# Kernel tuning notes

Hardware: AMD Instinct MI355X
Metric: run time of the kernel (lower is better)

Reference implementation:

```python
import jax, jax.numpy as jnp
import numpy as np

N = 12000   # nodes (multiple of 120)
E = 192000  # edges
T = 120     # utterances per dialogue
IN = 192
OUT = 6


def _edge_softmax(logits, dst, n):
    # logits: [E, H] -> softmax over incoming edges of each dst node
    m = jax.ops.segment_max(logits, dst, num_segments=n)
    ex = jnp.exp(logits - m[dst])
    s = jax.ops.segment_sum(ex, dst, num_segments=n)
    return ex / s[dst]


def _gatv2(h, src, dst, Wsrc, bsrc, Wdst, bdst, attn, Wres, n):
    # DGL GATv2Conv: e = attn . leakyrelu(fc_src(h)[u] + fc_dst(h)[v]), residual, relu activation
    Hh, F = attn.shape
    fs = (h @ Wsrc + bsrc).reshape(n, Hh, F)
    fd = (h @ Wdst + bdst).reshape(n, Hh, F)
    e = jax.nn.leaky_relu(fs[src] + fd[dst], 0.2)          # [E, H, F]
    logits = jnp.einsum('ehf,hf->eh', e, attn)              # [E, H]
    alpha = _edge_softmax(logits, dst, n)                   # [E, H]
    out = jax.ops.segment_sum(alpha[:, :, None] * fs[src], dst, num_segments=n)
    res = (h @ Wres).reshape(n, Hh, F)
    return jax.nn.relu(out + res)                           # [N, H, F]


def _lstm_dir(x, Wih, Whh, bih, bhh, reverse):
    # x: [T, B, D]; torch gate order i, f, g, o
    B = x.shape[1]
    hid = Whh.shape[1]
    def step(carry, xt):
        h, c = carry
        z = xt @ Wih.T + h @ Whh.T + bih + bhh
        i, f, g, o = jnp.split(z, 4, axis=-1)
        c = jax.nn.sigmoid(f) * c + jax.nn.sigmoid(i) * jnp.tanh(g)
        h = jax.nn.sigmoid(o) * jnp.tanh(c)
        return (h, c), h
    init = (jnp.zeros((B, hid), x.dtype), jnp.zeros((B, hid), x.dtype))
    _, hs = jax.lax.scan(step, init, x, reverse=reverse)
    return hs


def setup_inputs() -> dict:
    key = jax.random.key(0)
    ks = iter(jax.random.split(key, 64))
    def rn(shape, s=0.05):
        return jax.random.normal(next(ks), shape, jnp.float32) * s
    inp = {
        'text': rn((N, 1024), 1.0),
        'audio': rn((N, 512), 1.0),
        'vision': rn((N, 1024), 1.0),
        'edge_src': jax.random.randint(next(ks), (E,), 0, N, jnp.int32),
        'edge_dst': jax.random.randint(next(ks), (E,), 0, N, jnp.int32),
        # modality encoders
        'W_audio': rn((512, 64)), 'b_audio': jnp.zeros((64,), jnp.float32),
        'W_vision': rn((1024, 64)), 'b_vision': jnp.zeros((64,), jnp.float32),
        'W_text': rn((1024, 64)), 'b_text': jnp.zeros((64,), jnp.float32),
        # bidirectional LSTM (hidden=4 -> 16 gate rows)
        'Wih_f': rn((16, IN)), 'Whh_f': rn((16, 4)), 'bih_f': jnp.zeros((16,), jnp.float32), 'bhh_f': jnp.zeros((16,), jnp.float32),
        'Wih_b': rn((16, IN)), 'Whh_b': rn((16, 4)), 'bih_b': jnp.zeros((16,), jnp.float32), 'bhh_b': jnp.zeros((16,), jnp.float32),
        # imputation GraphConv (192->192, norm='both')
        'W_gc': rn((IN, IN)), 'b_gc': jnp.zeros((IN,), jnp.float32),
        # gat2 (cross-modal multi-head GAT, 192 -> 16 heads x 4)
        'Wsrc2': rn((IN, 64)), 'bsrc2': jnp.zeros((64,), jnp.float32),
        'Wdst2': rn((IN, 64)), 'bdst2': jnp.zeros((64,), jnp.float32),
        'attn2': rn((16, 4)), 'Wres2': rn((IN, 64)),
        # gat1 layer 0 (192 -> 16 heads x 32)
        'Wsrc0': rn((IN, 512)), 'bsrc0': jnp.zeros((512,), jnp.float32),
        'Wdst0': rn((IN, 512)), 'bdst0': jnp.zeros((512,), jnp.float32),
        'attn0': rn((16, 32)), 'Wres0': rn((IN, 512)),
        # gat1 layer 1 (512 -> 16 heads x 4)
        'Wsrc1': rn((512, 64)), 'bsrc1': jnp.zeros((64,), jnp.float32),
        'Wdst1': rn((512, 64)), 'bdst1': jnp.zeros((64,), jnp.float32),
        'attn1': rn((16, 4)), 'Wres1': rn((512, 64)),
        # final classifier Linear(136, out_size)
        'W_lin': rn((136, OUT)), 'b_lin': jnp.zeros((OUT,), jnp.float32),
    }
    return inp


def reference(text, audio, vision, edge_src, edge_dst,
              W_audio, b_audio, W_vision, b_vision, W_text, b_text,
              Wih_f, Whh_f, bih_f, bhh_f, Wih_b, Whh_b, bih_b, bhh_b,
              W_gc, b_gc,
              Wsrc2, bsrc2, Wdst2, bdst2, attn2, Wres2,
              Wsrc0, bsrc0, Wdst0, bdst0, attn0, Wres0,
              Wsrc1, bsrc1, Wdst1, bdst1, attn1, Wres1,
              W_lin, b_lin):
    n = text.shape[0]
    # modality encoders (dropout is identity at inference)
    t = text @ W_text + b_text
    a = audio @ W_audio + b_audio
    v = vision @ W_vision + b_vision
    stackFT = jnp.concatenate([t, a, v], axis=1)            # [N, 192]

    # bidirectional LSTM over dialogues of length T=120
    x = stackFT.reshape(-1, T, IN).transpose(1, 0, 2)       # [T, B, 192]
    hf = _lstm_dir(x, Wih_f, Whh_f, bih_f, bhh_f, False)
    hb = _lstm_dir(x, Wih_b, Whh_b, bih_b, bhh_b, True)
    newFeature = jnp.concatenate([hf, hb], -1).transpose(1, 0, 2).reshape(n, 8)

    # GraphConv imputation, norm='both' (degrees clamped to 1 as in DGL)
    ones = jnp.ones((edge_src.shape[0],), stackFT.dtype)
    deg_out = jnp.maximum(jax.ops.segment_sum(ones, edge_src, num_segments=n), 1.0)
    deg_in = jnp.maximum(jax.ops.segment_sum(ones, edge_dst, num_segments=n), 1.0)
    hw = (stackFT @ W_gc) * (deg_out ** -0.5)[:, None]
    h1 = jax.ops.segment_sum(hw[edge_src], edge_dst, num_segments=n) * (deg_in ** -0.5)[:, None] + b_gc
    h = 0.5 * (stackFT + h1)
    # F.normalize(h, p=1)
    h = h / jnp.maximum(jnp.sum(jnp.abs(h), axis=1, keepdims=True), 1e-12)

    # cross-modal multi-head GAT branch -> [N, 64]
    h3 = _gatv2(h, edge_src, edge_dst, Wsrc2, bsrc2, Wdst2, bdst2, attn2, Wres2, n).reshape(n, -1)

    # stacked GATv2 layers
    h = _gatv2(h, edge_src, edge_dst, Wsrc0, bsrc0, Wdst0, bdst0, attn0, Wres0, n).reshape(n, -1)  # [N, 512]
    h = _gatv2(h, edge_src, edge_dst, Wsrc1, bsrc1, Wdst1, bdst1, attn1, Wres1, n).reshape(n, -1)  # [N, 64]

    out = jnp.concatenate([h, newFeature, h3], axis=1) @ W_lin + b_lin  # [N, out_size]
    return out
```

## Files before the change

kernel.cpp:

```cpp
#include <hip/hip_runtime.h>

typedef __attribute__((ext_vector_type(8))) short short8;
typedef __attribute__((ext_vector_type(4))) float f32x4;

__device__ __forceinline__ unsigned short f2bf(float f) {
    unsigned u = __float_as_uint(f);
    u += 0x7FFFu + ((u >> 16) & 1u);
    return (unsigned short)(u >> 16);
}
__device__ __forceinline__ float bf2f(unsigned short h) {
    return __uint_as_float((unsigned)h << 16);
}

template<int MF, int OUTMODE>
__global__ __launch_bounds__(256)
void gemm_v6(const unsigned short* __restrict__ A, const float* __restrict__ B,
             const float* __restrict__ bias, const float* __restrict__ rowscale,
             void* __restrict__ Cv, const float* __restrict__ fin_num,
             const float* __restrict__ fin_den,
             int M, int Nb, int K, int ldc)
{
    __shared__ alignas(16) unsigned short As[MF * 64 * 32];
    __shared__ alignas(16) unsigned short Bs[4 * 64 * 8];
    const int t = threadIdx.x;
    const int w = t >> 6, l = t & 63;
    const int r16 = l & 15, kg = l >> 4;
    const int row0 = blockIdx.x * (64 * MF);
    const int col0 = blockIdx.y * 64;
    const int bcol = t & 63, bkg = t >> 6;

    f32x4 acc[MF][4] = {};
    const short8 z8 = {0, 0, 0, 0, 0, 0, 0, 0};

    for (int k0 = 0; k0 < K; k0 += 32) {
#pragma unroll
        for (int it = 0; it < MF; ++it) {
            int idx = it * 256 + t;
            int row = idx >> 2, ch = idx & 3;
            int gm = row0 + row;
            short8 v = z8;
            if (gm < M) v = *reinterpret_cast<const short8*>(A + (size_t)gm * K + k0 + ch * 8);
            *reinterpret_cast<short8*>(&As[row * 32 + ch * 8]) = v;
        }
        {
            const float* bp = B + (size_t)(k0 + bkg * 8) * Nb + col0 + bcol;
            short8 hv;
#pragma unroll
            for (int j = 0; j < 8; ++j) hv[j] = (short)f2bf(bp[(size_t)j * Nb]);
            *reinterpret_cast<short8*>(&Bs[bkg * 512 + bcol * 8]) = hv;
        }
        __syncthreads();
        short8 af[MF];
#pragma unroll
        for (int mi = 0; mi < MF; ++mi)
            af[mi] = *reinterpret_cast<const short8*>(&As[((w * MF + mi) * 16 + r16) * 32 + kg * 8]);
#pragma unroll
        for (int ni = 0; ni < 4; ++ni) {
            short8 bf = *reinterpret_cast<const short8*>(&Bs[kg * 512 + (ni * 16 + r16) * 8]);
#pragma unroll
            for (int mi = 0; mi < MF; ++mi)
                acc[mi][ni] = __builtin_amdgcn_mfma_f32_16x16x32_bf16(af[mi], bf, acc[mi][ni], 0, 0, 0);
        }
        __syncthreads();
    }
#pragma unroll
    for (int mi = 0; mi < MF; ++mi)
#pragma unroll
        for (int ni = 0; ni < 4; ++ni) {
            int col = col0 + ni * 16 + r16;
            float bv = bias ? bias[col] : 0.f;
#pragma unroll
            for (int r = 0; r < 4; ++r) {
                int gm = row0 + (w * MF + mi) * 16 + kg * 4 + r;
                if (gm < M) {
                    float val = acc[mi][ni][r] + bv;
                    if (rowscale) val *= rowscale[gm];
                    size_t idx = (size_t)gm * ldc + col;
                    if (OUTMODE == 0) {
                        ((float*)Cv)[idx] = val;
                    } else if (OUTMODE == 1) {
                        ((unsigned short*)Cv)[idx] = f2bf(val);
                    } else {
                        float d = fin_den[(size_t)gm * 16 + (col >> 5)];
                        float inv = (d > 0.f) ? __fdividef(1.f, d) : 0.f;
                        float o = fmaxf(fin_num[idx] * inv + val, 0.f);
                        ((unsigned short*)Cv)[idx] = f2bf(o);
                    }
                }
            }
        }
}

__global__ __launch_bounds__(256)
void enc_mfma3(const float* __restrict__ text, const float* __restrict__ audio, const float* __restrict__ vision,
               const float* __restrict__ Wt, const float* __restrict__ Wa, const float* __restrict__ Wv,
               const float* __restrict__ bt, const float* __restrict__ ba, const float* __restrict__ bv,
               float* __restrict__ Cf, unsigned short* __restrict__ Cb, int M)
{
    __shared__ alignas(16) unsigned short Ah[32 * 32], Ao[32 * 32];
    __shared__ alignas(16) unsigned short Bh[4 * 64 * 8], Bo[4 * 64 * 8];
    const int z = blockIdx.z;
    const float* A  = (z == 0) ? text : (z == 1) ? audio : vision;
    const float* W  = (z == 0) ? Wt   : (z == 1) ? Wa    : Wv;
    const float* bb = (z == 0) ? bt   : (z == 1) ? ba    : bv;
    const int K = (z == 1) ? 512 : 1024;

    const int t = threadIdx.x;
    const int w = t >> 6, l = t & 63;
    const int r16 = l & 15, kg = l >> 4;
    const int row0 = blockIdx.x * 32;
    const int mi = w & 1;
    const int ncol0 = (w >> 1) * 32;
    const int arow = t >> 3, ac8 = t & 7;
    const int bcol = t & 63, bkg = t >> 6;

    f32x4 acc[2] = {};
    for (int k0 = 0; k0 < K; k0 += 32) {
        {
            float4 av = *reinterpret_cast<const float4*>(A + (size_t)(row0 + arow) * K + k0 + ac8 * 4);
            float vv[4] = {av.x, av.y, av.z, av.w};
            ushort4 hi, lo;
            unsigned short* hp = (unsigned short*)&hi;
            unsigned short* lp = (unsigned short*)&lo;
#pragma unroll
            for (int j = 0; j < 4; ++j) {
                unsigned short h = f2bf(vv[j]);
                hp[j] = h;
                lp[j] = f2bf(vv[j] - bf2f(h));
            }
            *reinterpret_cast<ushort4*>(&Ah[arow * 32 + ac8 * 4]) = hi;
            *reinterpret_cast<ushort4*>(&Ao[arow * 32 + ac8 * 4]) = lo;
        }
        {
            const float* bp = W + (size_t)(k0 + bkg * 8) * 64 + bcol;
            short8 hv, lv;
#pragma unroll
            for (int j = 0; j < 8; ++j) {
                float x = bp[(size_t)j * 64];
                unsigned short h = f2bf(x);
                hv[j] = (short)h;
                lv[j] = (short)f2bf(x - bf2f(h));
            }
            *reinterpret_cast<short8*>(&Bh[bkg * 512 + bcol * 8]) = hv;
            *reinterpret_cast<short8*>(&Bo[bkg * 512 + bcol * 8]) = lv;
        }
        __syncthreads();
        short8 ah = *reinterpret_cast<const short8*>(&Ah[(mi * 16 + r16) * 32 + kg * 8]);
        short8 ao = *reinterpret_cast<const short8*>(&Ao[(mi * 16 + r16) * 32 + kg * 8]);
#pragma unroll
        for (int ni = 0; ni < 2; ++ni) {
            int ci = kg * 512 + (ncol0 + ni * 16 + r16) * 8;
            short8 bhv = *reinterpret_cast<const short8*>(&Bh[ci]);
            short8 bov = *reinterpret_cast<const short8*>(&Bo[ci]);
            acc[ni] = __builtin_amdgcn_mfma_f32_16x16x32_bf16(ah, bhv, acc[ni], 0, 0, 0);
            acc[ni] = __builtin_amdgcn_mfma_f32_16x16x32_bf16(ah, bov, acc[ni], 0, 0, 0);
            acc[ni] = __builtin_amdgcn_mfma_f32_16x16x32_bf16(ao, bhv, acc[ni], 0, 0, 0);
        }
        __syncthreads();
    }
#pragma unroll
    for (int ni = 0; ni < 2; ++ni) {
        int col = ncol0 + ni * 16 + r16;
        float bvv = bb[col];
#pragma unroll
        for (int r = 0; r < 4; ++r) {
            int gr = row0 + mi * 16 + kg * 4 + r;
            if (gr < M) {
                float val = acc[ni][r] + bvv;
                size_t idx = (size_t)gr * 192 + z * 64 + col;
                Cf[idx] = val;
                Cb[idx] = f2bf(val);
            }
        }
    }
}

__global__ void pack3_kernel(const float* __restrict__ W0, const float* __restrict__ W1, const float* __restrict__ W2,
                             const float* __restrict__ b0, const float* __restrict__ b1,
                             float* __restrict__ Wp, float* __restrict__ bp, int K, int O)
{
    int gid = blockIdx.x * blockDim.x + threadIdx.x;
    int O3 = 3 * O;
    if (gid < O3) bp[gid] = (gid < O) ? b0[gid] : (gid < 2 * O) ? b1[gid - O] : 0.f;
    if (gid >= K * O3) return;
    int k = gid / O3, c = gid - k * O3;
    float v = (c < O) ? W0[k * O + c] : (c < 2 * O) ? W1[k * O + c - O] : W2[k * O + c - 2 * O];
    Wp[gid] = v;
}

__global__ void pack2_kernel(const float* __restrict__ W0, const float* __restrict__ W1,
                             const float* __restrict__ b0, const float* __restrict__ b1,
                             float* __restrict__ Wp, float* __restrict__ bp, int K, int O)
{
    int gid = blockIdx.x * blockDim.x + threadIdx.x;
    int O2 = 2 * O;
    if (gid < O2) bp[gid] = (gid < O) ? b0[gid] : b1[gid - O];
    if (gid >= K * O2) return;
    int k = gid / O2, c = gid - k * O2;
    Wp[gid] = (c < O) ? W0[k * O + c] : W1[k * O + c - O];
}

__global__ void deg_kernel(const int* __restrict__ src, const int* __restrict__ dst,
                           int* degout, int* degin, int E)
{
    int e = blockIdx.x * blockDim.x + threadIdx.x;
    if (e < E) {
        atomicAdd(&degout[src[e]], 1);
        atomicAdd(&degin[dst[e]], 1);
    }
}

__global__ __launch_bounds__(1024)
void scan_kernel(const int* __restrict__ degin, int* __restrict__ rowstart, int n)
{
    __shared__ int part[1024];
    int t = threadIdx.x;
    int chunk = (n + 1023) / 1024;
    int s = 0;
    for (int i = 0; i < chunk; ++i) {
        int idx = t * chunk + i;
        if (idx < n) s += degin[idx];
    }
    part[t] = s;
    __syncthreads();
    for (int o = 1; o < 1024; o <<= 1) {
        int v = (t >= o) ? part[t - o] : 0;
        __syncthreads();
        part[t] += v;
        __syncthreads();
    }
    int run = (t > 0) ? part[t - 1] : 0;
    for (int i = 0; i < chunk; ++i) {
        int idx = t * chunk + i;
        if (idx < n) { rowstart[idx] = run; run += degin[idx]; }
    }
    if (t == 1023) rowstart[n] = part[1023];
}

__global__ void perm_kernel(const int* __restrict__ dst, const int* __restrict__ rowstart,
                            int* cursor, int* __restrict__ perm, int E)
{
    int e = blockIdx.x * blockDim.x + threadIdx.x;
    if (e < E) {
        int v = dst[e];
        int p = atomicAdd(&cursor[v], 1);
        perm[rowstart[v] + p] = e;
    }
}

__global__ void gather_src_kernel(const int* __restrict__ esrc, int* perm, int E)
{
    int i = blockIdx.x * blockDim.x + threadIdx.x;
    if (i < E) perm[i] = esrc[perm[i]];
}

__global__ void rs_kernel(const int* degout, const int* degin, float* rso, float* rsi, int n)
{
    int i = blockIdx.x * blockDim.x + threadIdx.x;
    if (i < n) {
        rso[i] = rsqrtf((float)max(degout[i], 1));
        rsi[i] = rsqrtf((float)max(degin[i], 1));
    }
}

__global__ void lstm_pre(const float* __restrict__ x, const float* __restrict__ Wf,
                         const float* __restrict__ Wb,
                         const float* bf1, const float* bf2, const float* bb1, const float* bb2,
                         float* __restrict__ xWf, float* __restrict__ xWb, int n)
{
    int gid = blockIdx.x * blockDim.x + threadIdx.x;
    if (gid >= n * 32) return;
    int nn = gid >> 5, r = gid & 31, d = r >> 4, j = r & 15;
    const float* W = (d ? Wb : Wf) + j * 192;
    const float* xr = x + (size_t)nn * 192;
    float s = 0.f;
#pragma unroll 4
    for (int k = 0; k < 192; k += 4) {
        float4 xv = *reinterpret_cast<const float4*>(xr + k);
        float4 wv = *reinterpret_cast<const float4*>(W + k);
        s += xv.x * wv.x + xv.y * wv.y + xv.z * wv.z + xv.w * wv.w;
    }
    s += d ? (bb1[j] + bb2[j]) : (bf1[j] + bf2[j]);
    int b = nn / 120, tt = nn - b * 120;
    (d ? xWb : xWf)[((size_t)b * 16 + j) * 120 + tt] = s;
}

__device__ __forceinline__ float fsigm(float x) { return __fdividef(1.f, 1.f + __expf(-x)); }
__device__ __forceinline__ float ftanh(float x) { return 1.f - __fdividef(2.f, __expf(2.f * x) + 1.f); }

template<int DIR>
__device__ void lstm_chain(const float* __restrict__ xw, const float* __restrict__ whh,
                           float* __restrict__ newF, int b)
{
    int j = threadIdx.x & 15;
    int k = j & 3;
    float4 w = *reinterpret_cast<const float4*>(whh + j * 4);
    const float* xp = xw + ((size_t)b * 16 + j) * 120;
    float h0 = 0.f, h1 = 0.f, h2 = 0.f, h3 = 0.f, cst = 0.f;
    int tb0 = DIR ? 108 : 0;
    float4 a0 = *reinterpret_cast<const float4*>(xp + tb0);
    float4 a1 = *reinterpret_cast<const float4*>(xp + tb0 + 4);
    float4 a2 = *reinterpret_cast<const float4*>(xp + tb0 + 8);
    for (int ch = 0; ch < 10; ++ch) {
        float4 b0 = a0, b1 = a1, b2 = a2;
        if (ch < 9) {
            int nt = DIR ? (96 - ch * 12) : (12 + ch * 12);
            b0 = *reinterpret_cast<const float4*>(xp + nt);
            b1 = *reinterpret_cast<const float4*>(xp + nt + 4);
            b2 = *reinterpret_cast<const float4*>(xp + nt + 8);
        }
        float zz[12] = {a0.x, a0.y, a0.z, a0.w, a1.x, a1.y, a1.z, a1.w, a2.x, a2.y, a2.z, a2.w};
        int tbase = DIR ? (108 - ch * 12) : (ch * 12);
#pragma unroll
        for (int ii = 0; ii < 12; ++ii) {
            int idx = DIR ? (11 - ii) : ii;
            float z = zz[idx] + ((w.x * h0 + w.y * h1) + (w.z * h2 + w.w * h3));
            float zi = __shfl(z, k, 16);
            float zf = __shfl(z, k + 4, 16);
            float zg = __shfl(z, k + 8, 16);
            float zo = __shfl(z, k + 12, 16);
            float ig = fsigm(zi), fg = fsigm(zf), gg = ftanh(zg), og = fsigm(zo);
            cst = fg * cst + ig * gg;
            float hn = og * ftanh(cst);
            h0 = __shfl(hn, 0, 16); h1 = __shfl(hn, 1, 16);
            h2 = __shfl(hn, 2, 16); h3 = __shfl(hn, 3, 16);
            if (j < 4) newF[((size_t)b * 120 + tbase + idx) * 8 + DIR * 4 + j] = hn;
        }
        a0 = b0; a1 = b1; a2 = b2;
    }
}

__global__ __launch_bounds__(64)
void lstm_seq2(const float* __restrict__ xWf, const float* __restrict__ xWb,
               const float* __restrict__ Whhf, const float* __restrict__ Whhb,
               float* __restrict__ newF, int B)
{
    int sub = threadIdx.x >> 4;
    int chain = blockIdx.x * 4 + sub;
    if (chain >= 2 * B) return;
    int d = chain / B;
    int b = chain - d * B;
    if (d == 0) lstm_chain<0>(xWf, Whhf, newF, b);
    else        lstm_chain<1>(xWb, Whhb, newF, b);
}

__global__ __launch_bounds__(256)
void gc_combine3(const float* __restrict__ stackFT, const float* __restrict__ hw,
                 const int* __restrict__ rowstart, const int* __restrict__ csrc,
                 const float* __restrict__ rs_in,
                 const float* __restrict__ b_gc, unsigned short* __restrict__ hB, int n)
{
    int v = blockIdx.x * 4 + (threadIdx.x >> 6);
    int l = threadIdx.x & 63;
    if (v >= n) return;
    int s0 = rowstart[v], s1 = rowstart[v + 1];
    float sum0 = 0.f, sum1 = 0.f, sum2 = 0.f;
    int u = (s0 < s1) ? csrc[s0] : 0;
    for (int i = s0; i < s1; ++i) {
        int un = (i + 1 < s1) ? csrc[i + 1] : 0;
        const float* hr = hw + (size_t)u * 192 + l;
        float p0 = hr[0], p1 = hr[64], p2 = hr[128];
        sum0 += p0; sum1 += p1; sum2 += p2;
        u = un;
    }
    float ri = rs_in[v];
    const float* sf = stackFT + (size_t)v * 192 + l;
    float v0 = 0.5f * (sf[0]   + sum0 * ri + b_gc[l]);
    float v1 = 0.5f * (sf[64]  + sum1 * ri + b_gc[l + 64]);
    float v2 = 0.5f * (sf[128] + sum2 * ri + b_gc[l + 128]);
    float r = fabsf(v0) + fabsf(v1) + fabsf(v2);
#pragma unroll
    for (int o = 32; o; o >>= 1) r += __shfl_xor(r, o);
    float inv = __fdividef(1.f, fmaxf(r, 1e-12f));
    unsigned short* hp = hB + (size_t)v * 192 + l;
    hp[0]   = f2bf(v0 * inv);
    hp[64]  = f2bf(v1 * inv);
    hp[128] = f2bf(v2 * inv);
}

__global__ __launch_bounds__(256)
void gat_edge4(const float* __restrict__ base, int ld,
               const float* __restrict__ attn,
               const int* __restrict__ rowstart, const int* __restrict__ csrc,
               float* __restrict__ outp, int n)
{
    int v = blockIdx.x * 16 + (threadIdx.x >> 4);
    int l = threadIdx.x & 15;
    if (v >= n) return;
    float4 at  = *reinterpret_cast<const float4*>(attn + l * 4);
    float4 fdv = *reinterpret_cast<const float4*>(base + (size_t)v * ld + 64 + l * 4);
    float4 acc = make_float4(0.f, 0.f, 0.f, 0.f);
    float dn = 0.f;
    int s0 = rowstart[v], s1 = rowstart[v + 1];
    int u = (s0 < s1) ? csrc[s0] : 0;
    float4 sv = (s0 < s1) ? *reinterpret_cast<const float4*>(base + (size_t)u * ld + l * 4)
                          : make_float4(0.f, 0.f, 0.f, 0.f);
    for (int i = s0; i < s1; ++i) {
        int un = (i + 1 < s1) ? csrc[i + 1] : 0;
        float4 svn = (i + 1 < s1) ? *reinterpret_cast<const float4*>(base + (size_t)un * ld + l * 4)
                                  : make_float4(0.f, 0.f, 0.f, 0.f);
        float ex_, ey, ez, ew;
        ex_ = sv.x + fdv.x; ex_ = (ex_ > 0.f) ? ex_ : 0.2f * ex_;
        ey  = sv.y + fdv.y; ey  = (ey  > 0.f) ? ey  : 0.2f * ey;
        ez  = sv.z + fdv.z; ez  = (ez  > 0.f) ? ez  : 0.2f * ez;
        ew  = sv.w + fdv.w; ew  = (ew  > 0.f) ? ew  : 0.2f * ew;
        float p = ex_ * at.x + ey * at.y + ez * at.z + ew * at.w;
        float ex = __expf(p);
        acc.x += ex * sv.x; acc.y += ex * sv.y; acc.z += ex * sv.z; acc.w += ex * sv.w;
        dn += ex;
        sv = svn; u = un;
    }
    float4 r = *reinterpret_cast<const float4*>(base + (size_t)v * ld + 128 + l * 4);
    float inv = (dn > 0.f) ? __fdividef(1.f, dn) : 0.f;
    float4 o;
    o.x = fmaxf(acc.x * inv + r.x, 0.f);
    o.y = fmaxf(acc.y * inv + r.y, 0.f);
    o.z = fmaxf(acc.z * inv + r.z, 0.f);
    o.w = fmaxf(acc.w * inv + r.w, 0.f);
    *reinterpret_cast<float4*>(outp + (size_t)v * 64 + l * 4) = o;
}

__global__ __launch_bounds__(256)
void gat_edge32(const unsigned short* __restrict__ base,
                const float* __restrict__ attn,
                const int* __restrict__ rowstart, const int* __restrict__ csrc,
                float* __restrict__ num, float* __restrict__ den, int n)
{
    int v = blockIdx.x * 2 + (threadIdx.x >> 7);
    int l = threadIdx.x & 127;
    if (v >= n) return;
    int head = l >> 3;
    float4 at = *reinterpret_cast<const float4*>(attn + head * 32 + (l & 7) * 4);
    ushort4 fdu = *reinterpret_cast<const ushort4*>(base + (size_t)v * 1024 + 512 + l * 4);
    float4 fdv = make_float4(bf2f(fdu.x), bf2f(fdu.y), bf2f(fdu.z), bf2f(fdu.w));
    float4 acc = make_float4(0.f, 0.f, 0.f, 0.f);
    float dn = 0.f;
    int s0 = rowstart[v], s1 = rowstart[v + 1];
    int u = (s0 < s1) ? csrc[s0] : 0;
    ushort4 su = (s0 < s1) ? *reinterpret_cast<const ushort4*>(base + (size_t)u * 1024 + l * 4)
                           : make_ushort4(0, 0, 0, 0);
    for (int i = s0; i < s1; ++i) {
        int un = (i + 1 < s1) ? csrc[i + 1] : 0;
        ushort4 sun = (i + 1 < s1) ? *reinterpret_cast<const ushort4*>(base + (size_t)un * 1024 + l * 4)
                                   : make_ushort4(0, 0, 0, 0);
        float4 sv = make_float4(bf2f(su.x), bf2f(su.y), bf2f(su.z), bf2f(su.w));
        float ex_, ey, ez, ew;
        ex_ = sv.x + fdv.x; ex_ = (ex_ > 0.f) ? ex_ : 0.2f * ex_;
        ey  = sv.y + fdv.y; ey  = (ey  > 0.f) ? ey  : 0.2f * ey;
        ez  = sv.z + fdv.z; ez  = (ez  > 0.f) ? ez  : 0.2f * ez;
        ew  = sv.w + fdv.w; ew  = (ew  > 0.f) ? ew  : 0.2f * ew;
        float p = ex_ * at.x + ey * at.y + ez * at.z + ew * at.w;
        p += __shfl_xor(p, 1, 8);
        p += __shfl_xor(p, 2, 8);
        p += __shfl_xor(p, 4, 8);
        float ex = __expf(p);
        acc.x += ex * sv.x; acc.y += ex * sv.y; acc.z += ex * sv.z; acc.w += ex * sv.w;
        dn += ex;
        su = sun; u = un;
    }
    *reinterpret_cast<float4*>(num + (size_t)v * 512 + l * 4) = acc;
    if ((l & 7) == 0) den[(size_t)v * 16 + head] = dn;
}

__global__ void final_lin(const float* __restrict__ h1, const float* __restrict__ newF,
                          const float* __restrict__ h3, const float* __restrict__ W,
                          const float* __restrict__ bias, float* __restrict__ out, int n)
{
    int gid = blockIdx.x * blockDim.x + threadIdx.x;
    if (gid >= n * 6) return;
    int v = gid / 6, o = gid - v * 6;
    float s = bias[o];
    const float* a = h1 + (size_t)v * 64;
#pragma unroll 8
    for (int r = 0; r < 64; ++r) s += a[r] * W[r * 6 + o];
    const float* b = newF + (size_t)v * 8;
#pragma unroll
    for (int r = 0; r < 8; ++r) s += b[r] * W[(64 + r) * 6 + o];
    const float* c = h3 + (size_t)v * 64;
#pragma unroll 8
    for (int r = 0; r < 64; ++r) s += c[r] * W[(72 + r) * 6 + o];
    out[gid] = s;
}

extern "C" void kernel_launch(void* const* d_in, const int* in_sizes, int n_in,
                              void* d_out, int out_size, void* d_ws, size_t ws_size,
                              hipStream_t stream)
{
    const float* text   = (const float*)d_in[0];
    const float* audio  = (const float*)d_in[1];
    const float* vision = (const float*)d_in[2];
    const int*   esrc   = (const int*)d_in[3];
    const int*   edst   = (const int*)d_in[4];
    const float* W_audio = (const float*)d_in[5];  const float* b_audio = (const float*)d_in[6];
    const float* W_vision= (const float*)d_in[7];  const float* b_vision= (const float*)d_in[8];
    const float* W_text  = (const float*)d_in[9];  const float* b_text  = (const float*)d_in[10];
    const float* Wih_f = (const float*)d_in[11]; const float* Whh_f = (const float*)d_in[12];
    const float* bih_f = (const float*)d_in[13]; const float* bhh_f = (const float*)d_in[14];
    const float* Wih_b = (const float*)d_in[15]; const float* Whh_b = (const float*)d_in[16];
    const float* bih_b = (const float*)d_in[17]; const float* bhh_b = (const float*)d_in[18];
    const float* W_gc  = (const float*)d_in[19]; const float* b_gc  = (const float*)d_in[20];
    const float* Wsrc2 = (const float*)d_in[21]; const float* bsrc2 = (const float*)d_in[22];
    const float* Wdst2 = (const float*)d_in[23]; const float* bdst2 = (const float*)d_in[24];
    const float* attn2 = (const float*)d_in[25]; const float* Wres2 = (const float*)d_in[26];
    const float* Wsrc0 = (const float*)d_in[27]; const float* bsrc0 = (const float*)d_in[28];
    const float* Wdst0 = (const float*)d_in[29]; const float* bdst0 = (const float*)d_in[30];
    const float* attn0 = (const float*)d_in[31]; const float* Wres0 = (const float*)d_in[32];
    const float* Wsrc1 = (const float*)d_in[33]; const float* bsrc1 = (const float*)d_in[34];
    const float* Wdst1 = (const float*)d_in[35]; const float* bdst1 = (const float*)d_in[36];
    const float* attn1 = (const float*)d_in[37]; const float* Wres1 = (const float*)d_in[38];
    const float* W_lin = (const float*)d_in[39]; const float* b_lin = (const float*)d_in[40];
    float* out = (float*)d_out;

    const int n = in_sizes[0] / 1024;
    const int E = in_sizes[3];
    const int B = n / 120;

    char* p = (char*)d_ws;
    auto alloc_f = [&](size_t cnt) { float* r = (float*)p; p += ((cnt * 4 + 255) / 256) * 256; return r; };
    auto alloc_h = [&](size_t cnt) { unsigned short* r = (unsigned short*)p; p += ((cnt * 2 + 255) / 256) * 256; return r; };
    auto alloc_i = [&](size_t cnt) { int* r = (int*)p; p += ((cnt * 4 + 255) / 256) * 256; return r; };
    float*          stackFT = alloc_f((size_t)n * 192);
    unsigned short* stackBF = alloc_h((size_t)n * 192);
    unsigned short* hbufBF  = alloc_h((size_t)n * 192);
    float* xWf     = alloc_f((size_t)n * 16);
    float* xWb     = alloc_f((size_t)n * 16);
    float* newF    = alloc_f((size_t)n * 8);
    float* big0    = alloc_f((size_t)n * 512);
    float* big1    = alloc_f((size_t)n * 512);
    float* big2    = alloc_f((size_t)n * 512);
    float* den     = alloc_f((size_t)n * 16);
    float* h3      = alloc_f((size_t)n * 64);
    float* h1s     = alloc_f((size_t)n * 64);
    float* rs_out  = alloc_f(n);
    float* rs_in   = alloc_f(n);
    int* zero_base = alloc_i((size_t)3 * n);
    int* degout = zero_base;
    int* degin  = zero_base + n;
    int* cursor = zero_base + 2 * n;
    int* rowstart = alloc_i((size_t)n + 1);
    int* perm     = alloc_i((size_t)E);
    if ((size_t)(p - (char*)d_ws) > ws_size) return;

    float* pw = h1s;
    float* pb = h1s + 200704;

    hipMemsetAsync(zero_base, 0, (size_t)3 * n * 4, stream);
    deg_kernel<<<(E + 255) / 256, 256, 0, stream>>>(esrc, edst, degout, degin, E);
    scan_kernel<<<1, 1024, 0, stream>>>(degin, rowstart, n);
    perm_kernel<<<(E + 255) / 256, 256, 0, stream>>>(edst, rowstart, cursor, perm, E);
    gather_src_kernel<<<(E + 255) / 256, 256, 0, stream>>>(esrc, perm, E);
    rs_kernel<<<(n + 255) / 256, 256, 0, stream>>>(degout, degin, rs_out, rs_in, n);
    const int* csrc = perm;

    auto gemm = [&](auto mf_tag, auto om_tag, const unsigned short* A, const float* Bm,
                    const float* bias, const float* rsc, void* Cp,
                    const float* fnum, const float* fden, int M, int Nb, int K, int ldc) {
        constexpr int MF = decltype(mf_tag)::value;
        constexpr int OM = decltype(om_tag)::value;
        dim3 grid((M + 64 * MF - 1) / (64 * MF), Nb / 64);
        gemm_v6<MF, OM><<<grid, 256, 0, stream>>>(A, Bm, bias, rsc, Cp, fnum, fden, M, Nb, K, ldc);
    };
    using I1 = std::integral_constant<int, 1>;
    using I2 = std::integral_constant<int, 2>;
    using O0 = std::integral_constant<int, 0>;
    using O1 = std::integral_constant<int, 1>;
    using O2 = std::integral_constant<int, 2>;

    {
        dim3 grid(n / 32, 1, 3);
        enc_mfma3<<<grid, 256, 0, stream>>>(text, audio, vision, W_text, W_audio, W_vision,
                                            b_text, b_audio, b_vision, stackFT, stackBF, n);
    }

    lstm_pre<<<(n * 32 + 255) / 256, 256, 0, stream>>>(stackFT, Wih_f, Wih_b,
                                                       bih_f, bhh_f, bih_b, bhh_b, xWf, xWb, n);
    lstm_seq2<<<(2 * B + 3) / 4, 64, 0, stream>>>(xWf, xWb, Whh_f, Whh_b, newF, B);

    gemm(I1{}, O0{}, stackBF, W_gc, nullptr, rs_out, big0, nullptr, nullptr, n, 192, 192, 192);
    gc_combine3<<<(n + 3) / 4, 256, 0, stream>>>(stackFT, big0, rowstart, csrc, rs_in, b_gc, hbufBF, n);

    pack3_kernel<<<(192 * 192 + 255) / 256, 256, 0, stream>>>(Wsrc2, Wdst2, Wres2, bsrc2, bdst2, pw, pb, 192, 64);
    gemm(I1{}, O0{}, hbufBF, pw, pb, nullptr, big0, nullptr, nullptr, n, 192, 192, 192);
    gat_edge4<<<(n + 15) / 16, 256, 0, stream>>>(big0, 192, attn2, rowstart, csrc, h3, n);

    pack2_kernel<<<(192 * 1024 + 255) / 256, 256, 0, stream>>>(Wsrc0, Wdst0, bsrc0, bdst0, pw, pb, 192, 512);
    gemm(I2{}, O1{}, hbufBF, pw, pb, nullptr, big0, nullptr, nullptr, n, 1024, 192, 1024);
    gat_edge32<<<(n + 1) / 2, 256, 0, stream>>>((const unsigned short*)big0, attn0, rowstart, csrc, big2, den, n);
    gemm(I1{}, O2{}, hbufBF, Wres0, nullptr, nullptr, big1, big2, den, n, 512, 192, 512);

    pack3_kernel<<<(512 * 192 + 255) / 256, 256, 0, stream>>>(Wsrc1, Wdst1, Wres1, bsrc1, bdst1, pw, pb, 512, 64);
    gemm(I1{}, O0{}, (const unsigned short*)big1, pw, pb, nullptr, big0, nullptr, nullptr, n, 192, 512, 192);
    gat_edge4<<<(n + 15) / 16, 256, 0, stream>>>(big0, 192, attn1, rowstart, csrc, h1s, n);

    final_lin<<<(n * 6 + 255) / 256, 256, 0, stream>>>(h1s, newF, h3, W_lin, b_lin, out, n);
}
```

Baseline: 397.4 us.

## Use fp16 single-pass encoder, bf16 pre-packed weights, register prefetch, bf16 intermediates

The modality encoder drops its three-MFMA bf16 hi/lo split and runs a single fp16 MFMA per tile, with encoder weights converted to fp16 once up front. GEMM weights are pre-converted to bf16 by pack kernels rather than converted on the fly inside every tile. Both GEMMs and the encoder now prefetch the next K-slice into registers while the current one computes. The 192-wide GEMM outputs are stored as bf16, halving gather traffic in the graph-conv and GAT edge kernels, at the cost of lower precision in the encoder and intermediates.

```diff
diff --git a/kernel.cpp b/kernel.cpp
--- a/kernel.cpp
+++ b/kernel.cpp
@@ -2,6 +2,8 @@
 
 typedef __attribute__((ext_vector_type(8))) short short8;
 typedef __attribute__((ext_vector_type(4))) float f32x4;
+typedef _Float16 half8v __attribute__((ext_vector_type(8)));
+typedef _Float16 half4v __attribute__((ext_vector_type(4)));
 
 __device__ __forceinline__ unsigned short f2bf(float f) {
     unsigned u = __float_as_uint(f);
@@ -14,7 +16,7 @@
 
 template<int MF, int OUTMODE>
 __global__ __launch_bounds__(256)
-void gemm_v6(const unsigned short* __restrict__ A, const float* __restrict__ B,
+void gemm_v7(const unsigned short* __restrict__ A, const unsigned short* __restrict__ B,
              const float* __restrict__ bias, const float* __restrict__ rowscale,
              void* __restrict__ Cv, const float* __restrict__ fin_num,
              const float* __restrict__ fin_den,
@@ -32,24 +34,45 @@
     f32x4 acc[MF][4] = {};
     const short8 z8 = {0, 0, 0, 0, 0, 0, 0, 0};
 
+    int srow[MF], sch[MF];
+    bool va[MF];
+    const unsigned short* aptr[MF];
+#pragma unroll
+    for (int it = 0; it < MF; ++it) {
+        int idx = it * 256 + t;
+        srow[it] = idx >> 2; sch[it] = idx & 3;
+        int gm = row0 + srow[it];
+        va[it] = gm < M;
+        aptr[it] = A + (size_t)gm * K + sch[it] * 8;
+    }
+    const unsigned short* bptr = B + (size_t)(bkg * 8) * Nb + col0 + bcol;
+
+    short8 pa[MF];
+    unsigned short pbv[8];
+#pragma unroll
+    for (int it = 0; it < MF; ++it)
+        pa[it] = va[it] ? *reinterpret_cast<const short8*>(aptr[it]) : z8;
+#pragma unroll
+    for (int j = 0; j < 8; ++j) pbv[j] = bptr[(size_t)j * Nb];
+
     for (int k0 = 0; k0 < K; k0 += 32) {
 #pragma unroll
-        for (int it = 0; it < MF; ++it) {
-            int idx = it * 256 + t;
-            int row = idx >> 2, ch = idx & 3;
-            int gm = row0 + row;
-            short8 v = z8;
-            if (gm < M) v = *reinterpret_cast<const short8*>(A + (size_t)gm * K + k0 + ch * 8);
-            *reinterpret_cast<short8*>(&As[row * 32 + ch * 8]) = v;
-        }
+        for (int it = 0; it < MF; ++it)
+            *reinterpret_cast<short8*>(&As[srow[it] * 32 + sch[it] * 8]) = pa[it];
         {
-            const float* bp = B + (size_t)(k0 + bkg * 8) * Nb + col0 + bcol;
             short8 hv;
 #pragma unroll
-            for (int j = 0; j < 8; ++j) hv[j] = (short)f2bf(bp[(size_t)j * Nb]);
+            for (int j = 0; j < 8; ++j) hv[j] = (short)pbv[j];
             *reinterpret_cast<short8*>(&Bs[bkg * 512 + bcol * 8]) = hv;
         }
         __syncthreads();
+        if (k0 + 32 < K) {
+#pragma unroll
+            for (int it = 0; it < MF; ++it)
+                pa[it] = va[it] ? *reinterpret_cast<const short8*>(aptr[it] + k0 + 32) : z8;
+#pragma unroll
+            for (int j = 0; j < 8; ++j) pbv[j] = bptr[(size_t)(k0 + 32 + j) * Nb];
+        }
         short8 af[MF];
 #pragma unroll
         for (int mi = 0; mi < MF; ++mi)
@@ -92,17 +115,17 @@
 }
 
 __global__ __launch_bounds__(256)
-void enc_mfma3(const float* __restrict__ text, const float* __restrict__ audio, const float* __restrict__ vision,
-               const float* __restrict__ Wt, const float* __restrict__ Wa, const float* __restrict__ Wv,
-               const float* __restrict__ bt, const float* __restrict__ ba, const float* __restrict__ bv,
-               float* __restrict__ Cf, unsigned short* __restrict__ Cb, int M)
-{
-    __shared__ alignas(16) unsigned short Ah[32 * 32], Ao[32 * 32];
-    __shared__ alignas(16) unsigned short Bh[4 * 64 * 8], Bo[4 * 64 * 8];
+void enc_f16(const float* __restrict__ text, const float* __restrict__ audio, const float* __restrict__ vision,
+             const _Float16* __restrict__ Wf16,
+             const float* __restrict__ bt, const float* __restrict__ ba, const float* __restrict__ bv,
+             float* __restrict__ Cf, unsigned short* __restrict__ Cb, int M)
+{
+    __shared__ alignas(16) _Float16 Af[32 * 32];
+    __shared__ alignas(16) _Float16 Bf[4 * 64 * 8];
     const int z = blockIdx.z;
     const float* A  = (z == 0) ? text : (z == 1) ? audio : vision;
-    const float* W  = (z == 0) ? Wt   : (z == 1) ? Wa    : Wv;
-    const float* bb = (z == 0) ? bt   : (z == 1) ? ba    : bv;
+    const _Float16* W = Wf16 + ((z == 0) ? 0 : (z == 1) ? 65536 : 98304);
+    const float* bb = (z == 0) ? bt : (z == 1) ? ba : bv;
     const int K = (z == 1) ? 512 : 1024;
 
     const int t = threadIdx.x;
@@ -114,47 +137,37 @@
     const int arow = t >> 3, ac8 = t & 7;
     const int bcol = t & 63, bkg = t >> 6;
 
+    const float* ap = A + (size_t)(row0 + arow) * K + ac8 * 4;
+    const _Float16* wp = W + (size_t)(bkg * 8) * 64 + bcol;
+
+    float4 pa = *reinterpret_cast<const float4*>(ap);
+    _Float16 pb[8];
+#pragma unroll
+    for (int j = 0; j < 8; ++j) pb[j] = wp[(size_t)j * 64];
+
     f32x4 acc[2] = {};
     for (int k0 = 0; k0 < K; k0 += 32) {
         {
-            float4 av = *reinterpret_cast<const float4*>(A + (size_t)(row0 + arow) * K + k0 + ac8 * 4);
-            float vv[4] = {av.x, av.y, av.z, av.w};
-            ushort4 hi, lo;
-            unsigned short* hp = (unsigned short*)&hi;
-            unsigned short* lp = (unsigned short*)&lo;
-#pragma unroll
-            for (int j = 0; j < 4; ++j) {
-                unsigned short h = f2bf(vv[j]);
-                hp[j] = h;
-                lp[j] = f2bf(vv[j] - bf2f(h));
-            }
-            *reinterpret_cast<ushort4*>(&Ah[arow * 32 + ac8 * 4]) = hi;
-            *reinterpret_cast<ushort4*>(&Ao[arow * 32 + ac8 * 4]) = lo;
-        }
-        {
-            const float* bp = W + (size_t)(k0 + bkg * 8) * 64 + bcol;
-            short8 hv, lv;
-#pragma unroll
-            for (int j = 0; j < 8; ++j) {
-                float x = bp[(size_t)j * 64];
-                unsigned short h = f2bf(x);
-                hv[j] = (short)h;
-                lv[j] = (short)f2bf(x - bf2f(h));
-            }
-            *reinterpret_cast<short8*>(&Bh[bkg * 512 + bcol * 8]) = hv;
-            *reinterpret_cast<short8*>(&Bo[bkg * 512 + bcol * 8]) = lv;
+            half4v av;
+            av[0] = (_Float16)pa.x; av[1] = (_Float16)pa.y;
+            av[2] = (_Float16)pa.z; av[3] = (_Float16)pa.w;
+            *reinterpret_cast<half4v*>(&Af[arow * 32 + ac8 * 4]) = av;
+            half8v bv8;
+#pragma unroll
+            for (int j = 0; j < 8; ++j) bv8[j] = pb[j];
+            *reinterpret_cast<half8v*>(&Bf[bkg * 512 + bcol * 8]) = bv8;
         }
         __syncthreads();
-        short8 ah = *reinterpret_cast<const short8*>(&Ah[(mi * 16 + r16) * 32 + kg * 8]);
-        short8 ao = *reinterpret_cast<const short8*>(&Ao[(mi * 16 + r16) * 32 + kg * 8]);
+        if (k0 + 32 < K) {
+            pa = *reinterpret_cast<const float4*>(ap + k0 + 32);
+#pragma unroll
+            for (int j = 0; j < 8; ++j) pb[j] = wp[(size_t)(k0 + 32 + j) * 64];
+        }
+        half8v af = *reinterpret_cast<const half8v*>(&Af[(mi * 16 + r16) * 32 + kg * 8]);
 #pragma unroll
         for (int ni = 0; ni < 2; ++ni) {
-            int ci = kg * 512 + (ncol0 + ni * 16 + r16) * 8;
-            short8 bhv = *reinterpret_cast<const short8*>(&Bh[ci]);
-            short8 bov = *reinterpret_cast<const short8*>(&Bo[ci]);
-            acc[ni] = __builtin_amdgcn_mfma_f32_16x16x32_bf16(ah, bhv, acc[ni], 0, 0, 0);
-            acc[ni] = __builtin_amdgcn_mfma_f32_16x16x32_bf16(ah, bov, acc[ni], 0, 0, 0);
-            acc[ni] = __builtin_amdgcn_mfma_f32_16x16x32_bf16(ao, bhv, acc[ni], 0, 0, 0);
+            half8v bf = *reinterpret_cast<const half8v*>(&Bf[kg * 512 + (ncol0 + ni * 16 + r16) * 8]);
+            acc[ni] = __builtin_amdgcn_mfma_f32_16x16x32_f16(af, bf, acc[ni], 0, 0, 0);
         }
         __syncthreads();
     }
@@ -175,9 +188,9 @@
     }
 }
 
-__global__ void pack3_kernel(const float* __restrict__ W0, const float* __restrict__ W1, const float* __restrict__ W2,
-                             const float* __restrict__ b0, const float* __restrict__ b1,
-                             float* __restrict__ Wp, float* __restrict__ bp, int K, int O)
+__global__ void pack3b(const float* __restrict__ W0, const float* __restrict__ W1, const float* __restrict__ W2,
+                       const float* __restrict__ b0, const float* __restrict__ b1,
+                       unsigned short* __restrict__ Wp, float* __restrict__ bp, int K, int O)
 {
     int gid = blockIdx.x * blockDim.x + threadIdx.x;
     int O3 = 3 * O;
@@ -185,19 +198,37 @@
     if (gid >= K * O3) return;
     int k = gid / O3, c = gid - k * O3;
     float v = (c < O) ? W0[k * O + c] : (c < 2 * O) ? W1[k * O + c - O] : W2[k * O + c - 2 * O];
-    Wp[gid] = v;
-}
-
-__global__ void pack2_kernel(const float* __restrict__ W0, const float* __restrict__ W1,
-                             const float* __restrict__ b0, const float* __restrict__ b1,
-                             float* __restrict__ Wp, float* __restrict__ bp, int K, int O)
+    Wp[gid] = f2bf(v);
+}
+
+__global__ void pack2b(const float* __restrict__ W0, const float* __restrict__ W1,
+                       const float* __restrict__ b0, const float* __restrict__ b1,
+                       unsigned short* __restrict__ Wp, float* __restrict__ bp, int K, int O)
 {
     int gid = blockIdx.x * blockDim.x + threadIdx.x;
     int O2 = 2 * O;
     if (gid < O2) bp[gid] = (gid < O) ? b0[gid] : b1[gid - O];
     if (gid >= K * O2) return;
     int k = gid / O2, c = gid - k * O2;
-    Wp[gid] = (c < O) ? W0[k * O + c] : W1[k * O + c - O];
+    Wp[gid] = f2bf((c < O) ? W0[k * O + c] : W1[k * O + c - O]);
+}
+
+__global__ void pack1b(const float* __restrict__ W, unsigned short* __restrict__ Wp, int cnt)
+{
+    int gid = blockIdx.x * blockDim.x + threadIdx.x;
+    if (gid < cnt) Wp[gid] = f2bf(W[gid]);
+}
+
+__global__ void pack_encw(const float* __restrict__ Wt, const float* __restrict__ Wa, const float* __restrict__ Wv,
+                          _Float16* __restrict__ out)
+{
+    int gid = blockIdx.x * blockDim.x + threadIdx.x;
+    if (gid >= 163840) return;
+    float v;
+    if (gid < 65536) v = Wt[gid];
+    else if (gid < 98304) v = Wa[gid - 65536];
+    else v = Wv[gid - 98304];
+    out[gid] = (_Float16)v;
 }
 
 __global__ void deg_kernel(const int* __restrict__ src, const int* __restrict__ dst,
@@ -345,7 +376,7 @@
 }
 
 __global__ __launch_bounds__(256)
-void gc_combine3(const float* __restrict__ stackFT, const float* __restrict__ hw,
+void gc_combine4(const float* __restrict__ stackFT, const unsigned short* __restrict__ hw,
                  const int* __restrict__ rowstart, const int* __restrict__ csrc,
                  const float* __restrict__ rs_in,
                  const float* __restrict__ b_gc, unsigned short* __restrict__ hB, int n)
@@ -358,9 +389,8 @@
     int u = (s0 < s1) ? csrc[s0] : 0;
     for (int i = s0; i < s1; ++i) {
         int un = (i + 1 < s1) ? csrc[i + 1] : 0;
-        const float* hr = hw + (size_t)u * 192 + l;
-        float p0 = hr[0], p1 = hr[64], p2 = hr[128];
-        sum0 += p0; sum1 += p1; sum2 += p2;
+        const unsigned short* hr = hw + (size_t)u * 192 + l;
+        sum0 += bf2f(hr[0]); sum1 += bf2f(hr[64]); sum2 += bf2f(hr[128]);
         u = un;
     }
     float ri = rs_in[v];
@@ -379,26 +409,28 @@
 }
 
 __global__ __launch_bounds__(256)
-void gat_edge4(const float* __restrict__ base, int ld,
-               const float* __restrict__ attn,
-               const int* __restrict__ rowstart, const int* __restrict__ csrc,
-               float* __restrict__ outp, int n)
+void gat_edge4b(const unsigned short* __restrict__ base,
+                const float* __restrict__ attn,
+                const int* __restrict__ rowstart, const int* __restrict__ csrc,
+                float* __restrict__ outp, int n)
 {
     int v = blockIdx.x * 16 + (threadIdx.x >> 4);
     int l = threadIdx.x & 15;
     if (v >= n) return;
-    float4 at  = *reinterpret_cast<const float4*>(attn + l * 4);
-    float4 fdv = *reinterpret_cast<const float4*>(base + (size_t)v * ld + 64 + l * 4);
+    float4 at = *reinterpret_cast<const float4*>(attn + l * 4);
+    ushort4 fdu = *reinterpret_cast<const ushort4*>(base + (size_t)v * 192 + 64 + l * 4);
+    float4 fdv = make_float4(bf2f(fdu.x), bf2f(fdu.y), bf2f(fdu.z), bf2f(fdu.w));
     float4 acc = make_float4(0.f, 0.f, 0.f, 0.f);
     float dn = 0.f;
     int s0 = rowstart[v], s1 = rowstart[v + 1];
     int u = (s0 < s1) ? csrc[s0] : 0;
-    float4 sv = (s0 < s1) ? *reinterpret_cast<const float4*>(base + (size_t)u * ld + l * 4)
-                          : make_float4(0.f, 0.f, 0.f, 0.f);
+    ushort4 su = (s0 < s1) ? *reinterpret_cast<const ushort4*>(base + (size_t)u * 192 + l * 4)
+                           : make_ushort4(0, 0, 0, 0);
     for (int i = s0; i < s1; ++i) {
         int un = (i + 1 < s1) ? csrc[i + 1] : 0;
-        float4 svn = (i + 1 < s1) ? *reinterpret_cast<const float4*>(base + (size_t)un * ld + l * 4)
-                                  : make_float4(0.f, 0.f, 0.f, 0.f);
+        ushort4 sun = (i + 1 < s1) ? *reinterpret_cast<const ushort4*>(base + (size_t)un * 192 + l * 4)
+                                   : make_ushort4(0, 0, 0, 0);
+        float4 sv = make_float4(bf2f(su.x), bf2f(su.y), bf2f(su.z), bf2f(su.w));
         float ex_, ey, ez, ew;
         ex_ = sv.x + fdv.x; ex_ = (ex_ > 0.f) ? ex_ : 0.2f * ex_;
         ey  = sv.y + fdv.y; ey  = (ey  > 0.f) ? ey  : 0.2f * ey;
@@ -408,15 +440,15 @@
         float ex = __expf(p);
         acc.x += ex * sv.x; acc.y += ex * sv.y; acc.z += ex * sv.z; acc.w += ex * sv.w;
         dn += ex;
-        sv = svn; u = un;
-    }
-    float4 r = *reinterpret_cast<const float4*>(base + (size_t)v * ld + 128 + l * 4);
+        su = sun; u = un;
+    }
+    ushort4 ru = *reinterpret_cast<const ushort4*>(base + (size_t)v * 192 + 128 + l * 4);
     float inv = (dn > 0.f) ? __fdividef(1.f, dn) : 0.f;
     float4 o;
-    o.x = fmaxf(acc.x * inv + r.x, 0.f);
-    o.y = fmaxf(acc.y * inv + r.y, 0.f);
-    o.z = fmaxf(acc.z * inv + r.z, 0.f);
-    o.w = fmaxf(acc.w * inv + r.w, 0.f);
+    o.x = fmaxf(acc.x * inv + bf2f(ru.x), 0.f);
+    o.y = fmaxf(acc.y * inv + bf2f(ru.y), 0.f);
+    o.z = fmaxf(acc.z * inv + bf2f(ru.z), 0.f);
+    o.w = fmaxf(acc.w * inv + bf2f(ru.w), 0.f);
     *reinterpret_cast<float4*>(outp + (size_t)v * 64 + l * 4) = o;
 }
 
@@ -522,6 +554,7 @@
     float*          stackFT = alloc_f((size_t)n * 192);
     unsigned short* stackBF = alloc_h((size_t)n * 192);
     unsigned short* hbufBF  = alloc_h((size_t)n * 192);
+    unsigned short* encW    = alloc_h(163840);
     float* xWf     = alloc_f((size_t)n * 16);
     float* xWb     = alloc_f((size_t)n * 16);
     float* newF    = alloc_f((size_t)n * 8);
@@ -541,8 +574,8 @@
     int* perm     = alloc_i((size_t)E);
     if ((size_t)(p - (char*)d_ws) > ws_size) return;
 
-    float* pw = h1s;
-    float* pb = h1s + 200704;
+    unsigned short* pw = (unsigned short*)h1s;
+    float* pb = h1s + 120000;
 
     hipMemsetAsync(zero_base, 0, (size_t)3 * n * 4, stream);
     deg_kernel<<<(E + 255) / 256, 256, 0, stream>>>(esrc, edst, degout, degin, E);
@@ -552,45 +585,48 @@
     rs_kernel<<<(n + 255) / 256, 256, 0, stream>>>(degout, degin, rs_out, rs_in, n);
     const int* csrc = perm;
 
-    auto gemm = [&](auto mf_tag, auto om_tag, const unsigned short* A, const float* Bm,
+    auto gemm = [&](auto mf_tag, auto om_tag, const unsigned short* A, const unsigned short* Bm,
                     const float* bias, const float* rsc, void* Cp,
                     const float* fnum, const float* fden, int M, int Nb, int K, int ldc) {
         constexpr int MF = decltype(mf_tag)::value;
         constexpr int OM = decltype(om_tag)::value;
         dim3 grid((M + 64 * MF - 1) / (64 * MF), Nb / 64);
-        gemm_v6<MF, OM><<<grid, 256, 0, stream>>>(A, Bm, bias, rsc, Cp, fnum, fden, M, Nb, K, ldc);
+        gemm_v7<MF, OM><<<grid, 256, 0, stream>>>(A, Bm, bias, rsc, Cp, fnum, fden, M, Nb, K, ldc);
     };
     using I1 = std::integral_constant<int, 1>;
     using I2 = std::integral_constant<int, 2>;
-    using O0 = std::integral_constant<int, 0>;
     using O1 = std::integral_constant<int, 1>;
     using O2 = std::integral_constant<int, 2>;
 
+    pack_encw<<<(163840 + 255) / 256, 256, 0, stream>>>(W_text, W_audio, W_vision, (_Float16*)encW);
     {
         dim3 grid(n / 32, 1, 3);
-        enc_mfma3<<<grid, 256, 0, stream>>>(text, audio, vision, W_text, W_audio, W_vision,
-                                            b_text, b_audio, b_vision, stackFT, stackBF, n);
+        enc_f16<<<grid, 256, 0, stream>>>(text, audio, vision, (const _Float16*)encW,
+                                          b_text, b_audio, b_vision, stackFT, stackBF, n);
     }
 
     lstm_pre<<<(n * 32 + 255) / 256, 256, 0, stream>>>(stackFT, Wih_f, Wih_b,
                                                        bih_f, bhh_f, bih_b, bhh_b, xWf, xWb, n);
     lstm_seq2<<<(2 * B + 3) / 4, 64, 0, stream>>>(xWf, xWb, Whh_f, Whh_b, newF, B);
 
-    gemm(I1{}, O0{}, stackBF, W_gc, nullptr, rs_out, big0, nullptr, nullptr, n, 192, 192, 192);
-    gc_combine3<<<(n + 3) / 4, 256, 0, stream>>>(stackFT, big0, rowstart, csrc, rs_in, b_gc, hbufBF, n);
-
-    pack3_kernel<<<(192 * 192 + 255) / 256, 256, 0, stream>>>(Wsrc2, Wdst2, Wres2, bsrc2, bdst2, pw, pb, 192, 64);
-    gemm(I1{}, O0{}, hbufBF, pw, pb, nullptr, big0, nullptr, nullptr, n, 192, 192, 192);
-    gat_edge4<<<(n + 15) / 16, 256, 0, stream>>>(big0, 192, attn2, rowstart, csrc, h3, n);
-
-    pack2_kernel<<<(192 * 1024 + 255) / 256, 256, 0, stream>>>(Wsrc0, Wdst0, bsrc0, bdst0, pw, pb, 192, 512);
+    pack1b<<<(192 * 192 + 255) / 256, 256, 0, stream>>>(W_gc, pw, 192 * 192);
+    gemm(I1{}, O1{}, stackBF, pw, nullptr, rs_out, big0, nullptr, nullptr, n, 192, 192, 192);
+    gc_combine4<<<(n + 3) / 4, 256, 0, stream>>>(stackFT, (const unsigned short*)big0,
+                                                 rowstart, csrc, rs_in, b_gc, hbufBF, n);
+
+    pack3b<<<(192 * 192 + 255) / 256, 256, 0, stream>>>(Wsrc2, Wdst2, Wres2, bsrc2, bdst2, pw, pb, 192, 64);
+    gemm(I1{}, O1{}, hbufBF, pw, pb, nullptr, big0, nullptr, nullptr, n, 192, 192, 192);
+    gat_edge4b<<<(n + 15) / 16, 256, 0, stream>>>((const unsigned short*)big0, attn2, rowstart, csrc, h3, n);
+
+    pack2b<<<(192 * 1024 + 255) / 256, 256, 0, stream>>>(Wsrc0, Wdst0, bsrc0, bdst0, pw, pb, 192, 512);
     gemm(I2{}, O1{}, hbufBF, pw, pb, nullptr, big0, nullptr, nullptr, n, 1024, 192, 1024);
     gat_edge32<<<(n + 1) / 2, 256, 0, stream>>>((const unsigned short*)big0, attn0, rowstart, csrc, big2, den, n);
-    gemm(I1{}, O2{}, hbufBF, Wres0, nullptr, nullptr, big1, big2, den, n, 512, 192, 512);
-
-    pack3_kernel<<<(512 * 192 + 255) / 256, 256, 0, stream>>>(Wsrc1, Wdst1, Wres1, bsrc1, bdst1, pw, pb, 512, 64);
-    gemm(I1{}, O0{}, (const unsigned short*)big1, pw, pb, nullptr, big0, nullptr, nullptr, n, 192, 512, 192);
-    gat_edge4<<<(n + 15) / 16, 256, 0, stream>>>(big0, 192, attn1, rowstart, csrc, h1s, n);
+    pack1b<<<(192 * 512 + 255) / 256, 256, 0, stream>>>(Wres0, pw, 192 * 512);
+    gemm(I1{}, O2{}, hbufBF, pw, nullptr, nullptr, big1, big2, den, n, 512, 192, 512);
+
+    pack3b<<<(512 * 192 + 255) / 256, 256, 0, stream>>>(Wsrc1, Wdst1, Wres1, bsrc1, bdst1, pw, pb, 512, 64);
+    gemm(I1{}, O1{}, (const unsigned short*)big1, pw, pb, nullptr, big0, nullptr, nullptr, n, 192, 512, 192);
+    gat_edge4b<<<(n + 15) / 16, 256, 0, stream>>>((const unsigned short*)big0, attn1, rowstart, csrc, h1s, n);
 
     final_lin<<<(n * 6 + 255) / 256, 256, 0, stream>>>(h1s, newF, h3, W_lin, b_lin, out, n);
 }
```

Measured after the change: 387.3 us. -2.6%, faster.
